# Performance work log

Hardware: AMD Instinct MI355X
Metric: run time of the kernel (lower is better)

Reference implementation:

```python
import jax, jax.numpy as jnp
import numpy as np

P, D, NF, NR, ND, EF, ER = 512, 128, 50000, 50000, 100000, 400000, 400000
BASELINE = 6.0


def setup_inputs() -> dict:
    key = jax.random.key(0)
    ctr = [0]
    def nk():
        ctr[0] += 1
        return jax.random.fold_in(key, ctr[0])
    def nrm(shape, scale=1.0):
        return jax.random.normal(nk(), shape, dtype=jnp.float32) * scale
    def uni(shape):
        return jax.random.uniform(nk(), shape, dtype=jnp.float32)
    def lin(fi, fo):
        return nrm((fi, fo), fi ** -0.5), jnp.zeros((fo,), jnp.float32)
    inp = {}
    inp['target_features'] = nrm((P,))
    inp['form_features'] = nrm((NF, P))
    inp['role_features'] = nrm((NR, P))
    inp['form_binds_y'] = BASELINE + nrm((EF,))
    inp['form_binds_w'] = uni((EF,))
    inp['role_binds_y'] = BASELINE + nrm((ER,))
    inp['role_binds_w'] = uni((ER,))
    inp['form_diff_w'] = uni((NF,)) + 0.01
    inp['role_diff_w'] = uni((NR,)) + 0.01
    inp['trust_vector'] = uni((3,))
    inp['drug_features'] = nrm((ND, D))
    inp['form_w1'], inp['form_b1'] = lin(P, P); inp['form_a1'] = jnp.full((1,), 0.25, jnp.float32)
    inp['form_w2'], inp['form_b2'] = lin(P, P)
    inp['role_w1'], inp['role_b1'] = lin(P, P); inp['role_a1'] = jnp.full((1,), 0.25, jnp.float32)
    inp['role_w2'], inp['role_b2'] = lin(P, P)
    inp['q_w'], inp['q_b'] = lin(P, D)
    inp['k_w'], inp['k_b'] = lin(D, D)
    inp['v_w'], inp['v_b'] = lin(D, D)
    inp['layer_emb'] = nrm((2, 16))
    inp['attn_w1'], inp['attn_b1'] = lin(2 * P + 16, 128)
    inp['attn_w2'], inp['attn_b2'] = lin(128, 64)
    inp['attn_w3'], inp['attn_b3'] = lin(64, 1)
    inp['mix_w1'], inp['mix_b1'] = lin(2 * D + 3, 64); inp['mix_a'] = jnp.full((1,), 0.25, jnp.float32)
    inp['mix_w2'], inp['mix_b2'] = lin(64, 2)
    inp['int_w1'], inp['int_b1'] = lin(D, P); inp['int_a'] = jnp.full((1,), 0.25, jnp.float32)
    inp['int_w2'], inp['int_b2'] = lin(P, P)
    inp['norm_w'] = jnp.ones((P,), jnp.float32)
    inp['norm_b'] = jnp.zeros((P,), jnp.float32)
    inp['delta_gate'] = jnp.float32(0.5)
    inp['form_neighbors'] = jnp.arange(NF, dtype=jnp.int32)
    inp['role_neighbors'] = jnp.arange(NR, dtype=jnp.int32)
    inp['form_binds_src'] = jax.random.randint(nk(), (EF,), 0, NF, dtype=jnp.int32)
    inp['form_binds_dst'] = jax.random.randint(nk(), (EF,), 0, ND, dtype=jnp.int32)
    inp['role_binds_src'] = jax.random.randint(nk(), (ER,), 0, NR, dtype=jnp.int32)
    inp['role_binds_dst'] = jax.random.randint(nk(), (ER,), 0, ND, dtype=jnp.int32)
    return inp


def _prelu(x, a):
    return jnp.where(x >= 0, x, a * x)


def _mlp2(x, w1, b1, a, w2, b2):
    return _prelu(x @ w1 + b1, a) @ w2 + b2


def _ln(x, w=None, b=None, eps=1e-5):
    m = jnp.mean(x, -1, keepdims=True)
    v = jnp.mean((x - m) ** 2, -1, keepdims=True)
    y = (x - m) * jax.lax.rsqrt(v + eps)
    return y if w is None else y * w + b


def _pref(z, nid, src, dst, y, w, drugs, q_w, q_b, k_w, k_b, v_w, v_b):
    # segment-softmax attention over (neighbor protein -> drug) bipartite edges
    N = nid.shape[0]
    order = jnp.argsort(nid)
    s = nid[order]
    pos = jnp.searchsorted(s, src)
    clip = jnp.minimum(pos, N - 1)
    valid = (pos < N) & (s[clip] == src)
    seg = jnp.where(valid, order[clip], N)  # invalid edges -> dump segment N
    q = z @ q_w + q_b                       # [D]
    d = drugs[dst]                          # [E, D] gather
    k = d @ k_w + k_b
    v = (d @ v_w + v_b) * ((y - BASELINE) * w)[:, None]
    logits = (k @ q) / (k.shape[-1] ** 0.5)
    mx = jax.ops.segment_max(logits, seg, num_segments=N + 1)
    mx = jnp.where(jnp.isfinite(mx), mx, 0.0)
    ex = jnp.where(valid, jnp.exp(logits - mx[seg]), 0.0)
    den = jax.ops.segment_sum(ex, seg, num_segments=N + 1) + 1e-12
    attn = ex / den[seg]
    return jax.ops.segment_sum(v * attn[:, None], seg, num_segments=N + 1)[:N]


def _attn_logits(z, zn, lemb, w1, b1, w2, b2, w3, b3):
    N = zn.shape[0]
    x = jnp.concatenate([jnp.broadcast_to(z, (N, z.shape[0])), zn,
                         jnp.broadcast_to(lemb, (N, lemb.shape[0]))], axis=-1)
    h = jax.nn.leaky_relu(x @ w1 + b1, 0.2)
    h = jax.nn.leaky_relu(h @ w2 + b2, 0.2)
    return (h @ w3 + b3)[:, 0]


def _core(fl, form_neighbors, role_neighbors, form_binds_src, form_binds_dst, role_binds_src, role_binds_dst):
    (target_features, form_features, role_features, form_binds_y, form_binds_w,
     role_binds_y, role_binds_w, form_diff_w, role_diff_w, trust_vector, drug_features,
     form_w1, form_b1, form_a1, form_w2, form_b2,
     role_w1, role_b1, role_a1, role_w2, role_b2,
     q_w, q_b, k_w, k_b, v_w, v_b, layer_emb,
     attn_w1, attn_b1, attn_w2, attn_b2, attn_w3, attn_b3,
     mix_w1, mix_b1, mix_a, mix_w2, mix_b2,
     int_w1, int_b1, int_a, int_w2, int_b2,
     norm_w, norm_b, delta_gate) = fl
    z_form = _mlp2(target_features, form_w1, form_b1, form_a1, form_w2, form_b2)
    z_role = _mlp2(target_features, role_w1, role_b1, role_a1, role_w2, role_b2)
    z = 0.5 * (z_form + z_role)
    form_feats = _mlp2(form_features, form_w1, form_b1, form_a1, form_w2, form_b2)
    role_feats = _mlp2(role_features, role_w1, role_b1, role_a1, role_w2, role_b2)
    form_msgs = _pref(z, form_neighbors, form_binds_src, form_binds_dst, form_binds_y, form_binds_w, drug_features, q_w, q_b, k_w, k_b, v_w, v_b)
    role_msgs = _pref(z, role_neighbors, role_binds_src, role_binds_dst, role_binds_y, role_binds_w, drug_features, q_w, q_b, k_w, k_b, v_w, v_b)
    form_logits = _attn_logits(z, form_feats, layer_emb[0], attn_w1, attn_b1, attn_w2, attn_b2, attn_w3, attn_b3)
    role_logits = _attn_logits(z, role_feats, layer_emb[1], attn_w1, attn_b1, attn_w2, attn_b2, attn_w3, attn_b3)
    form_attn = jax.nn.softmax(form_logits + jnp.log(jnp.maximum(form_diff_w, 1e-12)))
    role_attn = jax.nn.softmax(role_logits + jnp.log(jnp.maximum(role_diff_w, 1e-12)))
    v_form = form_attn @ form_msgs
    v_role = role_attn @ role_msgs
    mixer_in = jnp.concatenate([v_form, v_role, trust_vector])
    lw = jax.nn.softmax(_mlp2(mixer_in, mix_w1, mix_b1, mix_a, mix_w2, mix_b2))
    w_form, w_role = lw[0], lw[1]
    v_prior = w_form * v_form + w_role * v_role
    form_delta = form_attn @ (z[None, :] - form_feats)
    role_delta = role_attn @ (z[None, :] - role_feats)
    delta_raw = w_form * form_delta + w_role * role_delta
    delta_mean = delta_gate * _ln(delta_raw)
    z_refined = _ln(z + _mlp2(v_prior, int_w1, int_b1, int_a, int_w2, int_b2), norm_w, norm_b)
    return z_refined, v_prior, delta_mean


def reference(target_features, form_features, role_features, form_binds_y, form_binds_w, role_binds_y, role_binds_w, form_diff_w, role_diff_w, trust_vector, drug_features, form_w1, form_b1, form_a1, form_w2, form_b2, role_w1, role_b1, role_a1, role_w2, role_b2, q_w, q_b, k_w, k_b, v_w, v_b, layer_emb, attn_w1, attn_b1, attn_w2, attn_b2, attn_w3, attn_b3, mix_w1, mix_b1, mix_a, mix_w2, mix_b2, int_w1, int_b1, int_a, int_w2, int_b2, norm_w, norm_b, delta_gate, form_neighbors, role_neighbors, form_binds_src, form_binds_dst, role_binds_src, role_binds_dst):
    fl = (target_features, form_features, role_features, form_binds_y, form_binds_w,
          role_binds_y, role_binds_w, form_diff_w, role_diff_w, trust_vector, drug_features,
          form_w1, form_b1, form_a1, form_w2, form_b2,
          role_w1, role_b1, role_a1, role_w2, role_b2,
          q_w, q_b, k_w, k_b, v_w, v_b, layer_emb,
          attn_w1, attn_b1, attn_w2, attn_b2, attn_w3, attn_b3,
          mix_w1, mix_b1, mix_a, mix_w2, mix_b2,
          int_w1, int_b1, int_a, int_w2, int_b2,
          norm_w, norm_b, delta_gate)
    return _core(fl, form_neighbors, role_neighbors, form_binds_src, form_binds_dst, role_binds_src, role_binds_dst)
```

## Files before the change

### kernel.cpp

```cpp
#include <hip/hip_runtime.h>

#define NFN 50000
#define NDR 100000
#define NE  400000
#define MT  391
#define M0PAD 50048

__device__ __forceinline__ float bf2f(unsigned short u) {
    return __uint_as_float(((unsigned)u) << 16);
}
__device__ __forceinline__ unsigned short f2bf(float f) {
    unsigned u = __float_as_uint(f);
    unsigned r = 0x7FFFu + ((u >> 16) & 1u);
    return (unsigned short)((u + r) >> 16);
}
__device__ __forceinline__ unsigned bpack(float lo, float hi) {
    return (__float_as_uint(hi) & 0xFFFF0000u) | (__float_as_uint(lo) >> 16);
}

typedef __attribute__((ext_vector_type(8))) short bf16x8;
typedef __attribute__((ext_vector_type(4))) float f32x4;

struct KArgs {
    const float *tf, *ff, *rf, *fby, *fbw, *rby, *rbw, *fdw, *rdw, *trust, *drugs;
    const float *fw1, *fb1, *fa1, *fw2, *fb2, *rw1, *rb1, *ra1, *rw2, *rb2;
    const float *qw, *qb, *kw, *kb, *vw, *vb, *lemb;
    const float *aw1, *ab1, *aw2, *ab2, *aw3, *ab3;
    const float *mw1, *mb1, *ma, *mw2, *mb2;
    const float *iw1, *ib1, *ia, *iw2, *ib2;
    const float *nw, *nb, *dgate;
    const int *fsrc, *fdst, *rsrc, *rdst;
    float *shf, *shr;
    float *svf, *svr;
    float *gdenf, *gdenr;
    float *edenf, *edenr;
    float *cdf, *cdr;
    float *hraw;
    float *zraw;
    float *qraw;
    float *b1f, *b1r;
    float *sfr;
    float *o2raw;
    float *qk, *c0, *pe;
    unsigned short *w1tf, *w1tr;
    unsigned short *w2atf, *w2atr;
    unsigned short *aw2t;
    float *nexf, *nexr;
    unsigned short *H;
    float *hi;
    float *wfwr;
    float *out;
};

__global__ __launch_bounds__(512) void kA(KArgs A) {
    const int b = blockIdx.x;
    const int side = b >> 5, chunk = b & 31;
    const int tt = threadIdx.x;
    const float* w1 = side ? A.rw1 : A.fw1;
    float acc = 0.f;
    const int i0 = chunk * 16;
#pragma unroll
    for (int k = 0; k < 16; k++) {
        int i = i0 + k;
        acc = fmaf(A.tf[i], w1[(size_t)i * 512 + tt], acc);
    }
    atomicAdd(&A.hraw[side * 512 + tt], acc);
}

__global__ __launch_bounds__(512) void kB(KArgs A) {
    const int b = blockIdx.x;
    const int side = b >> 4, chunk = b & 15;
    const int tt = threadIdx.x;
    const float* w2 = side ? A.rw2 : A.fw2;
    const float* b1 = side ? A.rb1 : A.fb1;
    const float aa = (side ? A.ra1 : A.fa1)[0];
    float acc = 0.f;
    const int i0 = chunk * 32;
    for (int k = 0; k < 32; k++) {
        int i = i0 + k;
        float h = A.hraw[side * 512 + i] + b1[i];
        h = h >= 0.f ? h : aa * h;
        acc = fmaf(h, w2[(size_t)i * 512 + tt], acc);
    }
    if (b == 0) acc += A.fb2[tt] + A.rb2[tt];
    atomicAdd(&A.zraw[tt], acc);
}

__global__ __launch_bounds__(512) void kC1(KArgs A) {
    const int b = blockIdx.x;
    const int t = threadIdx.x;
    const int j = t & 127, isub = t >> 7;
    if (b < 8) {
        const int i0 = b * 64 + isub * 16;
        float acc = 0.f;
        for (int k = 0; k < 16; k++) {
            int i = i0 + k;
            acc = fmaf(0.5f * A.zraw[i], A.qw[(size_t)i * 128 + j], acc);
        }
        atomicAdd(&A.qraw[j], acc);
        if (b == 0 && t < 128) atomicAdd(&A.qraw[t], A.qb[t]);
    } else if (b < 16) {
        const int chunk = b - 8;
        const int i0 = chunk * 64 + isub * 16;
        float acc = 0.f;
        for (int k = 0; k < 16; k++) {
            int i = i0 + k;
            acc = fmaf(0.5f * A.zraw[i], A.aw1[(size_t)i * 128 + j], acc);
            acc = fmaf(A.fb2[i], A.aw1[(size_t)(512 + i) * 128 + j], acc);
        }
        atomicAdd(&A.b1f[j], acc);
        if (b == 8 && t < 128) {
            float c = A.ab1[t];
            for (int l = 0; l < 16; l++) c = fmaf(A.lemb[l], A.aw1[(size_t)(1024 + l) * 128 + t], c);
            atomicAdd(&A.b1f[t], c);
        }
    } else {
        const int chunk = b - 16;
        const int i0 = chunk * 64 + isub * 16;
        float acc = 0.f;
        for (int k = 0; k < 16; k++) {
            int i = i0 + k;
            acc = fmaf(0.5f * A.zraw[i], A.aw1[(size_t)i * 128 + j], acc);
            acc = fmaf(A.rb2[i], A.aw1[(size_t)(512 + i) * 128 + j], acc);
        }
        atomicAdd(&A.b1r[j], acc);
        if (b == 16 && t < 128) {
            float c = A.ab1[t];
            for (int l = 0; l < 16; l++) c = fmaf(A.lemb[16 + l], A.aw1[(size_t)(1024 + l) * 128 + t], c);
            atomicAdd(&A.b1r[t], c);
        }
    }
}

__global__ __launch_bounds__(256) void kC2(KArgs A) {
    const int t = threadIdx.x;
    __shared__ float sq[128];
    if (t < 128) sq[t] = A.qraw[t];
    __syncthreads();
    if (t < 128) {
        float s = 0.f;
        for (int j = 0; j < 128; j++) s = fmaf(A.kw[t * 128 + j], sq[j], s);
        A.qk[t] = s;
    } else if (t == 128) {
        float c = 0.f;
        for (int j = 0; j < 128; j++) c = fmaf(A.kb[j], sq[j], c);
        A.c0[0] = c;
    }
}

__global__ __launch_bounds__(512) void k_prep(KArgs A) {
    const int b = blockIdx.x;
    const int t = threadIdx.x;
    if (b < 128) {
        __shared__ float tl[64][65];
        const int side = b >> 6, tile = b & 63;
        const int k0 = (tile >> 3) * 64, n0 = (tile & 7) * 64;
        const float* w1 = side ? A.rw1 : A.fw1;
        unsigned short* o = side ? A.w1tr : A.w1tf;
        const int col = t & 63, rg = t >> 6;
#pragma unroll
        for (int i = 0; i < 8; i++) {
            const int row = rg * 8 + i;
            tl[row][col] = w1[(size_t)(k0 + row) * 512 + n0 + col];
        }
        __syncthreads();
#pragma unroll
        for (int i = 0; i < 8; i++) {
            const int nrow = rg * 8 + i;
            o[(size_t)(n0 + nrow) * 512 + k0 + col] = f2bf(tl[col][nrow]);
        }
    } else if (b < 384) {
        const int lb = b - 128;
        const int side = lb >> 7;
        const int i = (lb & 127) * 4 + (t >> 7);
        const int j = t & 127;
        const float* w2 = side ? A.rw2 : A.fw2;
        unsigned short* outp = side ? A.w2atr : A.w2atf;
        float s = 0.f;
        for (int k = 0; k < 512; k++)
            s = fmaf(w2[i * 512 + k], A.aw1[(size_t)(512 + k) * 128 + j], s);
        outp[(size_t)j * 512 + i] = f2bf(s);
    } else if (b < 400) {
        const int elem = (b - 384) * 512 + t;
        const int j = elem >> 7, i = elem & 127;
        A.aw2t[j * 128 + i] = f2bf(A.aw2[i * 64 + j]);
    } else {
        const int lane = t & 63;
        const int w = (b - 400) * 8 + (t >> 6);
        const float2 qk2 = *(const float2*)(A.qk + 2 * lane);
        const float c0 = A.c0[0];
        for (int dr = w; dr < NDR; dr += 2048) {
            float2 dv = *(const float2*)(A.drugs + (size_t)dr * 128 + 2 * lane);
            float p = fmaf(dv.x, qk2.x, dv.y * qk2.y);
            for (int off = 32; off >= 1; off >>= 1) p += __shfl_xor(p, off, 64);
            if (lane == 0) A.pe[dr] = expf((p + c0) * 0.088388347648318447f);
        }
    }
}

__global__ __launch_bounds__(256, 2)
void mfma_gemm(KArgs A) {
    __shared__ __align__(16) unsigned short Ab16[2][128 * 32];
    __shared__ __align__(16) unsigned short Bbuf[2][128 * 32];
    const int t = threadIdx.x;
    const int lane = t & 63, wv = t >> 6;
    const int p = blockIdx.x;
    const int L = (p & 7) * MT + (p >> 3);
    const int side = L >= (MT * 4);
    const int lbid = L - side * (MT * 4);
    const int m0l = (lbid >> 2) * 128, n0 = (lbid & 3) * 128;
    const float* __restrict__ Xf = side ? A.rf : A.ff;
    const unsigned short* __restrict__ Bt = side ? A.w1tr : A.w1tf;
    const float* __restrict__ bias = side ? A.rb1 : A.fb1;
    const float aval = (side ? A.ra1 : A.fa1)[0];
    unsigned short* __restrict__ Cv = A.H + (size_t)side * M0PAD * 512;
    const int wm = (wv >> 1) * 64, wn = (wv & 1) * 64;
    const int lm = lane & 15, ko = lane >> 4;
    const int K = 512;

    const int row0 = t >> 2, oct0 = t & 3;
    int ar0 = m0l + row0;       if (ar0 >= NFN) ar0 = NFN - 1;
    int ar1 = m0l + 64 + row0;  if (ar1 >= NFN) ar1 = NFN - 1;
    const float* __restrict__ asrc0 = Xf + (size_t)ar0 * K + oct0 * 8;
    const float* __restrict__ asrc1 = Xf + (size_t)ar1 * K + oct0 * 8;
    const int aslot0 = oct0 ^ ((row0 >> 1) & 3);
    const int aslot1 = oct0 ^ (((row0 + 64) >> 1) & 3);
    unsigned short* const adst0 = &(((unsigned short*)Ab16)[0]) ;

    f32x4 acc[4][4];
#pragma unroll
    for (int i = 0; i < 4; i++)
#pragma unroll
        for (int j = 0; j < 4; j++) acc[i][j] = (f32x4){0.f, 0.f, 0.f, 0.f};

    f32x4 rg[4];

    auto aload = [&](int k0) {
        rg[0] = *(const f32x4*)(asrc0 + k0);
        rg[1] = *(const f32x4*)(asrc0 + k0 + 4);
        rg[2] = *(const f32x4*)(asrc1 + k0);
        rg[3] = *(const f32x4*)(asrc1 + k0 + 4);
    };
    auto awrite = [&](int buf) {
        uint4 w0 = make_uint4(bpack(rg[0][0], rg[0][1]), bpack(rg[0][2], rg[0][3]),
                              bpack(rg[1][0], rg[1][1]), bpack(rg[1][2], rg[1][3]));
        uint4 w1 = make_uint4(bpack(rg[2][0], rg[2][1]), bpack(rg[2][2], rg[2][3]),
                              bpack(rg[3][0], rg[3][1]), bpack(rg[3][2], rg[3][3]));
        *(uint4*)&Ab16[buf][row0 * 32 + aslot0 * 8] = w0;
        *(uint4*)&Ab16[buf][(row0 + 64) * 32 + aslot1 * 8] = w1;
    };
    auto stageB = [&](int buf, int k0) {
#pragma unroll
        for (int ii = 0; ii < 2; ii++) {
            const int inst = wv * 2 + ii;
            const int rl = inst * 16 + (lane >> 2);
            const int sl = (lane & 3) ^ ((rl >> 1) & 3);
            __builtin_amdgcn_global_load_lds(
                (const __attribute__((address_space(1))) void*)(Bt + (size_t)(n0 + rl) * K + k0 + sl * 8),
                (__attribute__((address_space(3))) void*)(&Bbuf[buf][inst * 512]), 16, 0, 0);
        }
    };

    auto compute = [&](int buf) {
        bf16x8 af[4], bfr[4];
#pragma unroll
        for (int mi = 0; mi < 4; mi++) {
            int row = wm + mi * 16 + lm;
            af[mi] = *(const bf16x8*)&Ab16[buf][row * 32 + ((ko ^ ((row >> 1) & 3)) * 8)];
        }
#pragma unroll
        for (int ni = 0; ni < 4; ni++) {
            int col = wn + ni * 16 + lm;
            bfr[ni] = *(const bf16x8*)&Bbuf[buf][col * 32 + ((ko ^ ((col >> 1) & 3)) * 8)];
        }
#pragma unroll
        for (int mi = 0; mi < 4; mi++)
#pragma unroll
            for (int ni = 0; ni < 4; ni++)
                acc[mi][ni] = __builtin_amdgcn_mfma_f32_16x16x32_bf16(af[mi], bfr[ni], acc[mi][ni], 0, 0, 0);
    };

    aload(0);
    stageB(0, 0);
    awrite(0);
    __syncthreads();
    for (int kt = 0; kt < 16; kt++) {
        const int cur = kt & 1, nxt = cur ^ 1;
        if (kt + 1 < 16) {
            aload((kt + 1) * 32);
            stageB(nxt, (kt + 1) * 32);
        }
        compute(cur);
        if (kt + 1 < 16) awrite(nxt);
        __syncthreads();
    }

#pragma unroll
    for (int mi = 0; mi < 4; mi++) {
#pragma unroll
        for (int reg = 0; reg < 4; reg++) {
            int row = m0l + wm + mi * 16 + ko * 4 + reg;
#pragma unroll
            for (int ni = 0; ni < 4; ni++) {
                int col = n0 + wn + ni * 16 + lm;
                float v = acc[mi][ni][reg] + bias[col];
                v = v >= 0.f ? v : aval * v;
                Cv[(size_t)row * 512 + col] = f2bf(v);
            }
        }
    }
}

__global__ __launch_bounds__(256, 2)
void gemm_logits(KArgs A) {
    __shared__ __align__(16) unsigned short Abuf[2][128 * 32];
    __shared__ __align__(16) unsigned short Bbuf[2][128 * 32];
    __shared__ __align__(16) unsigned short Gs[128][136];
    __shared__ float ps[128];
    __shared__ float red2[128];
    __shared__ float snex[128];
    const int bid = blockIdx.x;
    const int side = bid >= MT;
    const int m0l = (bid - side * MT) * 128;
    const unsigned short* __restrict__ Ab = A.H + (size_t)side * M0PAD * 512;
    const unsigned short* __restrict__ Bt = side ? A.w2atr : A.w2atf;
    const float* __restrict__ bias = side ? A.b1r : A.b1f;
    const float* __restrict__ dw = side ? A.rdw : A.fdw;
    float* __restrict__ nex = side ? A.nexr : A.nexf;
    float* __restrict__ gden = side ? A.gdenr : A.gdenf;
    const int t = threadIdx.x;
    const int lane = t & 63, wv = t >> 6;
    const int wm = (wv >> 1) * 64, wn = (wv & 1) * 64;
    const int lm = lane & 15, ko = lane >> 4;
    const int K = 512;

    f32x4 acc[4][4];
#pragma unroll
    for (int i = 0; i < 4; i++)
#pragma unroll
        for (int j = 0; j < 4; j++) acc[i][j] = (f32x4){0.f, 0.f, 0.f, 0.f};

    auto stage = [&](int buf, int k0) {
#pragma unroll
        for (int ii = 0; ii < 2; ii++) {
            const int inst = wv * 2 + ii;
            const int rl = inst * 16 + (lane >> 2);
            const int sl = (lane & 3) ^ ((rl >> 1) & 3);
            int ar = m0l + rl; if (ar >= NFN) ar = NFN - 1;
            __builtin_amdgcn_global_load_lds(
                (const __attribute__((address_space(1))) void*)(Ab + (size_t)ar * K + k0 + sl * 8),
                (__attribute__((address_space(3))) void*)(&Abuf[buf][inst * 512]), 16, 0, 0);
            __builtin_amdgcn_global_load_lds(
                (const __attribute__((address_space(1))) void*)(Bt + (size_t)rl * K + k0 + sl * 8),
                (__attribute__((address_space(3))) void*)(&Bbuf[buf][inst * 512]), 16, 0, 0);
        }
    };

    auto compute = [&](int buf) {
        bf16x8 af[4], bfr[4];
#pragma unroll
        for (int mi = 0; mi < 4; mi++) {
            int row = wm + mi * 16 + lm;
            af[mi] = *(const bf16x8*)&Abuf[buf][row * 32 + ((ko ^ ((row >> 1) & 3)) * 8)];
        }
#pragma unroll
        for (int ni = 0; ni < 4; ni++) {
            int col = wn + ni * 16 + lm;
            bfr[ni] = *(const bf16x8*)&Bbuf[buf][col * 32 + ((ko ^ ((col >> 1) & 3)) * 8)];
        }
#pragma unroll
        for (int mi = 0; mi < 4; mi++)
#pragma unroll
            for (int ni = 0; ni < 4; ni++)
                acc[mi][ni] = __builtin_amdgcn_mfma_f32_16x16x32_bf16(af[mi], bfr[ni], acc[mi][ni], 0, 0, 0);
    };

    stage(0, 0);
    __syncthreads();
    for (int kt = 0; kt < 16; kt++) {
        if (kt + 1 < 16) stage((kt + 1) & 1, (kt + 1) * 32);
        compute(kt & 1);
        __syncthreads();
    }

#pragma unroll
    for (int mi = 0; mi < 4; mi++) {
#pragma unroll
        for (int reg = 0; reg < 4; reg++) {
            int row_l = wm + mi * 16 + ko * 4 + reg;
#pragma unroll
            for (int ni = 0; ni < 4; ni++) {
                int col = wn + ni * 16 + lm;
                float v = acc[mi][ni][reg] + bias[col];
                v = v >= 0.f ? v : 0.2f * v;
                Gs[row_l][col] = f2bf(v);
            }
        }
    }
    __syncthreads();

    const int wr0 = wv * 32;
    float ab2v[4], aw3v[4];
#pragma unroll
    for (int ni = 0; ni < 4; ni++) {
        int col = ni * 16 + lm;
        ab2v[ni] = A.ab2[col];
        aw3v[ni] = A.aw3[col];
    }
    f32x4 acc2[2][4];
#pragma unroll
    for (int i = 0; i < 2; i++)
#pragma unroll
        for (int j = 0; j < 4; j++) acc2[i][j] = (f32x4){0.f, 0.f, 0.f, 0.f};
#pragma unroll
    for (int kk = 0; kk < 4; kk++) {
        bf16x8 ga[2], bb[4];
#pragma unroll
        for (int mi = 0; mi < 2; mi++)
            ga[mi] = *(const bf16x8*)&Gs[wr0 + mi * 16 + lm][kk * 32 + ko * 8];
#pragma unroll
        for (int ni = 0; ni < 4; ni++)
            bb[ni] = *(const bf16x8*)(A.aw2t + (size_t)(ni * 16 + lm) * 128 + kk * 32 + ko * 8);
#pragma unroll
        for (int mi = 0; mi < 2; mi++)
#pragma unroll
            for (int ni = 0; ni < 4; ni++)
                acc2[mi][ni] = __builtin_amdgcn_mfma_f32_16x16x32_bf16(ga[mi], bb[ni], acc2[mi][ni], 0, 0, 0);
    }
#pragma unroll
    for (int mi = 0; mi < 2; mi++) {
#pragma unroll
        for (int reg = 0; reg < 4; reg++) {
            float s = 0.f;
#pragma unroll
            for (int ni = 0; ni < 4; ni++) {
                float v = acc2[mi][ni][reg] + ab2v[ni];
                v = v >= 0.f ? v : 0.2f * v;
                s = fmaf(v, aw3v[ni], s);
            }
            s += __shfl_xor(s, 1, 64);
            s += __shfl_xor(s, 2, 64);
            s += __shfl_xor(s, 4, 64);
            s += __shfl_xor(s, 8, 64);
            if (lm == 0) ps[wr0 + mi * 16 + ko * 4 + reg] = s;
        }
    }
    __syncthreads();
    float val = 0.f;
    if (t < 128) {
        int node = m0l + t;
        if (node < NFN) {
            val = expf(ps[t] + A.ab3[0] + logf(fmaxf(dw[node], 1e-12f)));
            nex[node] = val;
        }
        snex[t] = val;
        red2[t] = val;
    }
    __syncthreads();
    if (t < 64) red2[t] += red2[t + 64];
    __syncthreads();
    if (t < 32) red2[t] += red2[t + 32];
    __syncthreads();
    if (t < 16) red2[t] += red2[t + 16];
    __syncthreads();
    if (t == 0) {
        float s = 0.f;
        for (int i = 0; i < 16; i++) s += red2[i];
        atomicAdd(gden, s);
    }
    {
        const unsigned short* Hrow = Ab + (size_t)m0l * 512;
        float a0 = 0.f, a1 = 0.f;
        for (int r = 0; r < 128; r += 2) {
            const float w0 = snex[r], w1 = snex[r + 1];
            const unsigned v0 = *(const unsigned*)(Hrow + (size_t)r * 512 + 2 * t);
            const unsigned v1 = *(const unsigned*)(Hrow + (size_t)(r + 1) * 512 + 2 * t);
            a0 = fmaf(w0, bf2f((unsigned short)(v0 & 0xFFFFu)), a0);
            a1 = fmaf(w0, bf2f((unsigned short)(v0 >> 16)), a1);
            a0 = fmaf(w1, bf2f((unsigned short)(v1 & 0xFFFFu)), a0);
            a1 = fmaf(w1, bf2f((unsigned short)(v1 >> 16)), a1);
        }
        float* SH = side ? A.shr : A.shf;
        atomicAdd(&SH[2 * t], a0);
        atomicAdd(&SH[2 * t + 1], a1);
    }
}

__global__ __launch_bounds__(256) void k_edge1(KArgs A) {
    const int side = blockIdx.y;
    const int* src = side ? A.rsrc : A.fsrc;
    const int* dst = side ? A.rdst : A.fdst;
    float* eden = side ? A.edenr : A.edenf;
    const int base = blockIdx.x * 2048 + threadIdx.x;
#pragma unroll
    for (int u = 0; u < 8; u++) {
        const int e = base + u * 256;
        if (e < NE) atomicAdd(&eden[src[e]], A.pe[dst[e]]);
    }
}

__global__ __launch_bounds__(256) void k_nfac(KArgs A) {
    const int side = blockIdx.y;
    const int n = blockIdx.x * 256 + threadIdx.x;
    if (n >= NFN) return;
    const float* nex = side ? A.nexr : A.nexf;
    float* eden = side ? A.edenr : A.edenf;
    const float invden = 1.0f / *(side ? A.gdenr : A.gdenf);
    eden[n] = nex[n] * invden / (eden[n] + 1e-12f);
}

__global__ __launch_bounds__(256) void k_edge2(KArgs A) {
    const int side = blockIdx.y;
    const int* src = side ? A.rsrc : A.fsrc;
    const int* dst = side ? A.rdst : A.fdst;
    const float* yy = side ? A.rby : A.fby;
    const float* ww = side ? A.rbw : A.fbw;
    const float* fac = side ? A.edenr : A.edenf;
    float* cd = side ? A.cdr : A.cdf;
    float* sv = side ? A.svr : A.svf;
    const int base = blockIdx.x * 2048 + threadIdx.x;
    float csum = 0.f;
#pragma unroll
    for (int u = 0; u < 8; u++) {
        const int e = base + u * 256;
        if (e < NE) {
            float coef = fac[src[e]] * A.pe[dst[e]] * ((yy[e] - 6.0f) * ww[e]);
            atomicAdd(&cd[dst[e]], coef);
            csum += coef;
        }
    }
    __shared__ float red[256];
    red[threadIdx.x] = csum; __syncthreads();
    for (int s2 = 128; s2 >= 1; s2 >>= 1) {
        if (threadIdx.x < s2) red[threadIdx.x] += red[threadIdx.x + s2];
        __syncthreads();
    }
    if (threadIdx.x == 0) atomicAdd(&sv[128], red[0]);
}

__global__ __launch_bounds__(256) void k_wsumD(KArgs A) {
    const int t = threadIdx.x;
    const int col = t & 127, rg = t >> 7;
    __shared__ float red[2][2][128];
    float af = 0.f, ar = 0.f;
    for (int dr = blockIdx.x * 2 + rg; dr < NDR; dr += gridDim.x * 2) {
        float cf = A.cdf[dr], cr = A.cdr[dr];
        float dv = A.drugs[(size_t)dr * 128 + col];
        af = fmaf(cf, dv, af);
        ar = fmaf(cr, dv, ar);
    }
    red[rg][0][col] = af; red[rg][1][col] = ar;
    __syncthreads();
    if (rg == 0) {
        atomicAdd(&A.svf[col], red[0][0][col] + red[1][0][col]);
        atomicAdd(&A.svr[col], red[0][1][col] + red[1][1][col]);
    }
}

__global__ __launch_bounds__(512) void kF12(KArgs A) {
    const int b = blockIdx.x;
    const int t = threadIdx.x;
    if (b < 16) {
        const int side = b >> 3, chunk = b & 7;
        const float* w2 = side ? A.rw2 : A.fw2;
        const float* SH = side ? A.shr : A.shf;
        const float invden = 1.0f / *(side ? A.gdenr : A.gdenf);
        float acc = 0.f;
        const int i0 = chunk * 64;
        for (int k = 0; k < 64; k++) {
            int i = i0 + k;
            acc = fmaf(SH[i], w2[(size_t)i * 512 + t], acc);
        }
        acc *= invden;
        if (chunk == 0) acc += (side ? A.rb2 : A.fb2)[t];
        atomicAdd(&A.sfr[side * 512 + t], acc);
        return;
    }
    __shared__ float vform[128], vrole[128], vprior[128], mh[64], sw[2];
    if (t < 128) {
        float vf = A.svf[128] * A.vb[t];
        float vr = A.svr[128] * A.vb[t];
        for (int i = 0; i < 128; i++) {
            vf = fmaf(A.svf[i], A.vw[i * 128 + t], vf);
            vr = fmaf(A.svr[i], A.vw[i * 128 + t], vr);
        }
        vform[t] = vf; vrole[t] = vr;
    }
    __syncthreads();
    if (t < 64) {
        float m = A.mb1[t];
        for (int i = 0; i < 128; i++) m = fmaf(vform[i], A.mw1[i * 64 + t], m);
        for (int i = 0; i < 128; i++) m = fmaf(vrole[i], A.mw1[(128 + i) * 64 + t], m);
        for (int i = 0; i < 3; i++)   m = fmaf(A.trust[i], A.mw1[(256 + i) * 64 + t], m);
        float ma = A.ma[0];
        mh[t] = m >= 0.f ? m : ma * m;
    }
    __syncthreads();
    if (t < 2) {
        float o = A.mb2[t];
        for (int i = 0; i < 64; i++) o = fmaf(mh[i], A.mw2[i * 2 + t], o);
        sw[t] = o;
    }
    __syncthreads();
    const float mo = fmaxf(sw[0], sw[1]);
    const float e0 = expf(sw[0] - mo), e1 = expf(sw[1] - mo);
    const float wf = e0 / (e0 + e1), wr = e1 / (e0 + e1);
    if (t == 0) { A.wfwr[0] = wf; A.wfwr[1] = wr; }
    if (t < 128) {
        float vp = wf * vform[t] + wr * vrole[t];
        vprior[t] = vp;
        A.out[512 + t] = vp;
    }
    __syncthreads();
    float hi = A.ib1[t];
    for (int i = 0; i < 128; i++) hi = fmaf(vprior[i], A.iw1[(size_t)i * 512 + t], hi);
    float ia = A.ia[0];
    A.hi[t] = hi >= 0.f ? hi : ia * hi;
}

__global__ __launch_bounds__(512) void kF3(KArgs A) {
    const int chunk = blockIdx.x;
    const int tt = threadIdx.x;
    float acc = 0.f;
    const int i0 = chunk * 64;
    for (int k = 0; k < 64; k++) {
        int i = i0 + k;
        acc = fmaf(A.hi[i], A.iw2[(size_t)i * 512 + tt], acc);
    }
    if (chunk == 0) acc += A.ib2[tt];
    atomicAdd(&A.o2raw[tt], acc);
}

__global__ __launch_bounds__(512) void kF4(KArgs A) {
    const int t = threadIdx.x;
    __shared__ float red[512];
    const float wf = A.wfwr[0], wr = A.wfwr[1];
    const float zv = 0.5f * A.zraw[t];
    float dr_ = zv - wf * A.sfr[t] - wr * A.sfr[512 + t];
    red[t] = dr_; __syncthreads();
    for (int s = 256; s >= 1; s >>= 1) { if (t < s) red[t] += red[t + s]; __syncthreads(); }
    float mean = red[0] * (1.f / 512.f); __syncthreads();
    float dd = dr_ - mean;
    red[t] = dd * dd; __syncthreads();
    for (int s = 256; s >= 1; s >>= 1) { if (t < s) red[t] += red[t + s]; __syncthreads(); }
    float var = red[0] * (1.f / 512.f); __syncthreads();
    A.out[640 + t] = A.dgate[0] * (dd * rsqrtf(var + 1e-5f));
    float zin = zv + A.o2raw[t];
    red[t] = zin; __syncthreads();
    for (int s = 256; s >= 1; s >>= 1) { if (t < s) red[t] += red[t + s]; __syncthreads(); }
    float mean2 = red[0] * (1.f / 512.f); __syncthreads();
    float d2 = zin - mean2;
    red[t] = d2 * d2; __syncthreads();
    for (int s = 256; s >= 1; s >>= 1) { if (t < s) red[t] += red[t + s]; __syncthreads(); }
    float var2 = red[0] * (1.f / 512.f);
    A.out[t] = (d2 * rsqrtf(var2 + 1e-5f)) * A.nw[t] + A.nb[t];
}

extern "C" void kernel_launch(void* const* d_in, const int* in_sizes, int n_in,
                              void* d_out, int out_size, void* d_ws, size_t ws_size,
                              hipStream_t stream) {
    (void)in_sizes; (void)n_in; (void)out_size;
    KArgs A;
    A.tf    = (const float*)d_in[0];
    A.ff    = (const float*)d_in[1];
    A.rf    = (const float*)d_in[2];
    A.fby   = (const float*)d_in[3];
    A.fbw   = (const float*)d_in[4];
    A.rby   = (const float*)d_in[5];
    A.rbw   = (const float*)d_in[6];
    A.fdw   = (const float*)d_in[7];
    A.rdw   = (const float*)d_in[8];
    A.trust = (const float*)d_in[9];
    A.drugs = (const float*)d_in[10];
    A.fw1 = (const float*)d_in[11]; A.fb1 = (const float*)d_in[12]; A.fa1 = (const float*)d_in[13];
    A.fw2 = (const float*)d_in[14]; A.fb2 = (const float*)d_in[15];
    A.rw1 = (const float*)d_in[16]; A.rb1 = (const float*)d_in[17]; A.ra1 = (const float*)d_in[18];
    A.rw2 = (const float*)d_in[19]; A.rb2 = (const float*)d_in[20];
    A.qw = (const float*)d_in[21]; A.qb = (const float*)d_in[22];
    A.kw = (const float*)d_in[23]; A.kb = (const float*)d_in[24];
    A.vw = (const float*)d_in[25]; A.vb = (const float*)d_in[26];
    A.lemb = (const float*)d_in[27];
    A.aw1 = (const float*)d_in[28]; A.ab1 = (const float*)d_in[29];
    A.aw2 = (const float*)d_in[30]; A.ab2 = (const float*)d_in[31];
    A.aw3 = (const float*)d_in[32]; A.ab3 = (const float*)d_in[33];
    A.mw1 = (const float*)d_in[34]; A.mb1 = (const float*)d_in[35]; A.ma = (const float*)d_in[36];
    A.mw2 = (const float*)d_in[37]; A.mb2 = (const float*)d_in[38];
    A.iw1 = (const float*)d_in[39]; A.ib1 = (const float*)d_in[40]; A.ia = (const float*)d_in[41];
    A.iw2 = (const float*)d_in[42]; A.ib2 = (const float*)d_in[43];
    A.nw = (const float*)d_in[44]; A.nb = (const float*)d_in[45];
    A.dgate = (const float*)d_in[46];
    A.fsrc = (const int*)d_in[49];
    A.fdst = (const int*)d_in[50];
    A.rsrc = (const int*)d_in[51];
    A.rdst = (const int*)d_in[52];
    A.out = (float*)d_out;

    char* w = (char*)d_ws;
    size_t off = 0;
    auto alloc = [&](size_t bytes) -> void* {
        void* p = w + off;
        off = (off + bytes + 255) & ~(size_t)255;
        return p;
    };
    A.shf   = (float*)alloc(512 * 4);
    A.shr   = (float*)alloc(512 * 4);
    A.svf   = (float*)alloc(129 * 4);
    A.svr   = (float*)alloc(129 * 4);
    A.gdenf = (float*)alloc(4);
    A.gdenr = (float*)alloc(4);
    A.edenf = (float*)alloc((size_t)NFN * 4);
    A.edenr = (float*)alloc((size_t)NFN * 4);
    A.cdf   = (float*)alloc((size_t)NDR * 4);
    A.cdr   = (float*)alloc((size_t)NDR * 4);
    A.hraw  = (float*)alloc(1024 * 4);
    A.zraw  = (float*)alloc(512 * 4);
    A.qraw  = (float*)alloc(128 * 4);
    A.b1f   = (float*)alloc(128 * 4);
    A.b1r   = (float*)alloc(128 * 4);
    A.sfr   = (float*)alloc(1024 * 4);
    A.o2raw = (float*)alloc(512 * 4);
    const size_t zbytes = off;
    A.qk   = (float*)alloc(128 * 4);
    A.c0   = (float*)alloc(4);
    A.pe   = (float*)alloc((size_t)NDR * 4);
    A.w1tf = (unsigned short*)alloc((size_t)512 * 512 * 2);
    A.w1tr = (unsigned short*)alloc((size_t)512 * 512 * 2);
    A.w2atf = (unsigned short*)alloc((size_t)128 * 512 * 2);
    A.w2atr = (unsigned short*)alloc((size_t)128 * 512 * 2);
    A.aw2t  = (unsigned short*)alloc((size_t)64 * 128 * 2);
    A.nexf  = (float*)alloc((size_t)NFN * 4);
    A.nexr  = (float*)alloc((size_t)NFN * 4);
    A.H     = (unsigned short*)alloc((size_t)2 * M0PAD * 512 * 2);
    A.hi    = (float*)alloc(512 * 4);
    A.wfwr  = (float*)alloc(2 * 4);
    if (ws_size && off > ws_size) return;

    hipMemsetAsync(d_ws, 0, zbytes, stream);

    kA<<<64, 512, 0, stream>>>(A);
    kB<<<32, 512, 0, stream>>>(A);
    kC1<<<24, 512, 0, stream>>>(A);
    kC2<<<1, 256, 0, stream>>>(A);
    k_prep<<<656, 512, 0, stream>>>(A);

    const int EB8 = (NE + 2047) / 2048;
    const int NFB = (NFN + 255) / 256;
    mfma_gemm<<<2 * MT * 4, 256, 0, stream>>>(A);
    gemm_logits<<<2 * MT, 256, 0, stream>>>(A);
    k_edge1<<<dim3(EB8, 2), 256, 0, stream>>>(A);
    k_nfac<<<dim3(NFB, 2), 256, 0, stream>>>(A);
    k_edge2<<<dim3(EB8, 2), 256, 0, stream>>>(A);
    k_wsumD<<<512, 256, 0, stream>>>(A);
    kF12<<<17, 512, 0, stream>>>(A);
    kF3<<<8, 512, 0, stream>>>(A);
    kF4<<<1, 512, 0, stream>>>(A);
}
```

Baseline: 435.6 us.

## Prefetch GEMM tiles two stages ahead via registers, replace direct-to-LDS B loads

The first-layer MLP GEMM now prefetches A and B tiles two k-steps ahead into two alternating register sets, writing the next stage to LDS after compute. B is loaded through registers with the same swizzled layout as A instead of using global_load_lds. The aim is to hide more global memory latency behind MFMA work, at the cost of extra VGPRs that could lower occupancy.

```diff
diff --git a/kernel.cpp b/kernel.cpp
--- a/kernel.cpp
+++ b/kernel.cpp
@@ -223,9 +223,10 @@
     int ar1 = m0l + 64 + row0;  if (ar1 >= NFN) ar1 = NFN - 1;
     const float* __restrict__ asrc0 = Xf + (size_t)ar0 * K + oct0 * 8;
     const float* __restrict__ asrc1 = Xf + (size_t)ar1 * K + oct0 * 8;
-    const int aslot0 = oct0 ^ ((row0 >> 1) & 3);
-    const int aslot1 = oct0 ^ (((row0 + 64) >> 1) & 3);
-    unsigned short* const adst0 = &(((unsigned short*)Ab16)[0]) ;
+    const unsigned short* __restrict__ bsrc0 = Bt + (size_t)(n0 + row0) * K + oct0 * 8;
+    const unsigned short* __restrict__ bsrc1 = Bt + (size_t)(n0 + 64 + row0) * K + oct0 * 8;
+    const int slot0 = oct0 ^ ((row0 >> 1) & 3);
+    const int slot1 = oct0 ^ (((row0 + 64) >> 1) & 3);
 
     f32x4 acc[4][4];
 #pragma unroll
@@ -233,32 +234,52 @@
 #pragma unroll
         for (int j = 0; j < 4; j++) acc[i][j] = (f32x4){0.f, 0.f, 0.f, 0.f};
 
-    f32x4 rg[4];
-
-    auto aload = [&](int k0) {
-        rg[0] = *(const f32x4*)(asrc0 + k0);
-        rg[1] = *(const f32x4*)(asrc0 + k0 + 4);
-        rg[2] = *(const f32x4*)(asrc1 + k0);
-        rg[3] = *(const f32x4*)(asrc1 + k0 + 4);
-    };
-    auto awrite = [&](int buf) {
-        uint4 w0 = make_uint4(bpack(rg[0][0], rg[0][1]), bpack(rg[0][2], rg[0][3]),
-                              bpack(rg[1][0], rg[1][1]), bpack(rg[1][2], rg[1][3]));
-        uint4 w1 = make_uint4(bpack(rg[2][0], rg[2][1]), bpack(rg[2][2], rg[2][3]),
-                              bpack(rg[3][0], rg[3][1]), bpack(rg[3][2], rg[3][3]));
-        *(uint4*)&Ab16[buf][row0 * 32 + aslot0 * 8] = w0;
-        *(uint4*)&Ab16[buf][(row0 + 64) * 32 + aslot1 * 8] = w1;
-    };
-    auto stageB = [&](int buf, int k0) {
-#pragma unroll
-        for (int ii = 0; ii < 2; ii++) {
-            const int inst = wv * 2 + ii;
-            const int rl = inst * 16 + (lane >> 2);
-            const int sl = (lane & 3) ^ ((rl >> 1) & 3);
-            __builtin_amdgcn_global_load_lds(
-                (const __attribute__((address_space(1))) void*)(Bt + (size_t)(n0 + rl) * K + k0 + sl * 8),
-                (__attribute__((address_space(3))) void*)(&Bbuf[buf][inst * 512]), 16, 0, 0);
-        }
+    f32x4 pa0[4], pa1[4];
+    uint4 pb0[2], pb1[2];
+
+    auto aload0 = [&](int k0) {
+        pa0[0] = *(const f32x4*)(asrc0 + k0);
+        pa0[1] = *(const f32x4*)(asrc0 + k0 + 4);
+        pa0[2] = *(const f32x4*)(asrc1 + k0);
+        pa0[3] = *(const f32x4*)(asrc1 + k0 + 4);
+    };
+    auto aload1 = [&](int k0) {
+        pa1[0] = *(const f32x4*)(asrc0 + k0);
+        pa1[1] = *(const f32x4*)(asrc0 + k0 + 4);
+        pa1[2] = *(const f32x4*)(asrc1 + k0);
+        pa1[3] = *(const f32x4*)(asrc1 + k0 + 4);
+    };
+    auto bload0 = [&](int k0) {
+        pb0[0] = *(const uint4*)(bsrc0 + k0);
+        pb0[1] = *(const uint4*)(bsrc1 + k0);
+    };
+    auto bload1 = [&](int k0) {
+        pb1[0] = *(const uint4*)(bsrc0 + k0);
+        pb1[1] = *(const uint4*)(bsrc1 + k0);
+    };
+    auto awrite0 = [&](int buf) {
+        uint4 w0 = make_uint4(bpack(pa0[0][0], pa0[0][1]), bpack(pa0[0][2], pa0[0][3]),
+                              bpack(pa0[1][0], pa0[1][1]), bpack(pa0[1][2], pa0[1][3]));
+        uint4 w1 = make_uint4(bpack(pa0[2][0], pa0[2][1]), bpack(pa0[2][2], pa0[2][3]),
+                              bpack(pa0[3][0], pa0[3][1]), bpack(pa0[3][2], pa0[3][3]));
+        *(uint4*)&Ab16[buf][row0 * 32 + slot0 * 8] = w0;
+        *(uint4*)&Ab16[buf][(row0 + 64) * 32 + slot1 * 8] = w1;
+    };
+    auto awrite1 = [&](int buf) {
+        uint4 w0 = make_uint4(bpack(pa1[0][0], pa1[0][1]), bpack(pa1[0][2], pa1[0][3]),
+                              bpack(pa1[1][0], pa1[1][1]), bpack(pa1[1][2], pa1[1][3]));
+        uint4 w1 = make_uint4(bpack(pa1[2][0], pa1[2][1]), bpack(pa1[2][2], pa1[2][3]),
+                              bpack(pa1[3][0], pa1[3][1]), bpack(pa1[3][2], pa1[3][3]));
+        *(uint4*)&Ab16[buf][row0 * 32 + slot0 * 8] = w0;
+        *(uint4*)&Ab16[buf][(row0 + 64) * 32 + slot1 * 8] = w1;
+    };
+    auto bwrite0 = [&](int buf) {
+        *(uint4*)&Bbuf[buf][row0 * 32 + slot0 * 8] = pb0[0];
+        *(uint4*)&Bbuf[buf][(row0 + 64) * 32 + slot1 * 8] = pb0[1];
+    };
+    auto bwrite1 = [&](int buf) {
+        *(uint4*)&Bbuf[buf][row0 * 32 + slot0 * 8] = pb1[0];
+        *(uint4*)&Bbuf[buf][(row0 + 64) * 32 + slot1 * 8] = pb1[1];
     };
 
     auto compute = [&](int buf) {
@@ -280,18 +301,21 @@
                 acc[mi][ni] = __builtin_amdgcn_mfma_f32_16x16x32_bf16(af[mi], bfr[ni], acc[mi][ni], 0, 0, 0);
     };
 
-    aload(0);
-    stageB(0, 0);
-    awrite(0);
+    aload0(0); bload0(0);
+    awrite0(0); bwrite0(0);
+    aload1(32); bload1(32);
     __syncthreads();
     for (int kt = 0; kt < 16; kt++) {
         const int cur = kt & 1, nxt = cur ^ 1;
+        if (kt + 2 < 16) {
+            if ((kt & 1) == 0) { aload0((kt + 2) * 32); bload0((kt + 2) * 32); }
+            else               { aload1((kt + 2) * 32); bload1((kt + 2) * 32); }
+        }
+        compute(cur);
         if (kt + 1 < 16) {
-            aload((kt + 1) * 32);
-            stageB(nxt, (kt + 1) * 32);
-        }
-        compute(cur);
-        if (kt + 1 < 16) awrite(nxt);
+            if (((kt + 1) & 1) == 0) { awrite0(nxt); bwrite0(nxt); }
+            else                     { awrite1(nxt); bwrite1(nxt); }
+        }
         __syncthreads();
     }
 
```

Measured after the change: 540.3 us. +24.0%, slower.
